# Performance work log

Measured on AMD Instinct MI355X. Metric: run time of the kernel, lower is better.

Reference implementation:

```python
import jax, jax.numpy as jnp
import numpy as np

N_NODES = 100000
N_EDGES = 1600000
HIDDEN = 128
N_ETYPES = 4
N_STEPS = 4


def setup_inputs() -> dict:
    key = jax.random.key(0)
    ks = jax.random.split(key, 10)
    s = 1.0 / np.sqrt(HIDDEN)
    node_feat = jax.random.normal(ks[0], (N_NODES, HIDDEN), dtype=jnp.float32)
    edge_index = jax.random.randint(ks[1], (2, N_EDGES), 0, N_NODES)
    edge_feat = jax.random.uniform(ks[2], (N_EDGES, N_ETYPES), dtype=jnp.float32)
    # per-edge-type linear layers (DGL GatedGraphConv uses nn.Linear per etype)
    W_edge = jax.random.uniform(ks[3], (N_ETYPES, HIDDEN, HIDDEN), minval=-s, maxval=s, dtype=jnp.float32)
    b_edge = jax.random.uniform(ks[4], (N_ETYPES, HIDDEN), minval=-s, maxval=s, dtype=jnp.float32)
    # GRUCell parameters (torch layout: gates stacked r, z, n)
    W_ih = jax.random.uniform(ks[5], (3 * HIDDEN, HIDDEN), minval=-s, maxval=s, dtype=jnp.float32)
    W_hh = jax.random.uniform(ks[6], (3 * HIDDEN, HIDDEN), minval=-s, maxval=s, dtype=jnp.float32)
    b_ih = jax.random.uniform(ks[7], (3 * HIDDEN,), minval=-s, maxval=s, dtype=jnp.float32)
    b_hh = jax.random.uniform(ks[8], (3 * HIDDEN,), minval=-s, maxval=s, dtype=jnp.float32)
    return {"node_feat": node_feat, "edge_index": edge_index, "edge_feat": edge_feat,
            "W_edge": W_edge, "b_edge": b_edge, "W_ih": W_ih, "W_hh": W_hh,
            "b_ih": b_ih, "b_hh": b_hh}


def _gru_cell(x, h, W_ih, W_hh, b_ih, b_hh):
    gi = x @ W_ih.T + b_ih  # (N, 3D)
    gh = h @ W_hh.T + b_hh
    ir, iz, inn = jnp.split(gi, 3, axis=1)
    hr, hz, hn = jnp.split(gh, 3, axis=1)
    r = jax.nn.sigmoid(ir + hr)
    z = jax.nn.sigmoid(iz + hz)
    n = jnp.tanh(inn + r * hn)
    return (1.0 - z) * n + z * h


def reference(node_feat, edge_index, edge_feat, W_edge, b_edge, W_ih, W_hh, b_ih, b_hh):
    etypes = jnp.argmax(edge_feat, axis=1)          # (E,)
    src, dst = edge_index[0], edge_index[1]
    N = node_feat.shape[0]
    h = node_feat
    for _ in range(N_STEPS):
        # per-etype linear transform of all nodes: (T, N, D)
        trans = jnp.einsum('nd,tod->tno', h, W_edge) + b_edge[:, None, :]
        msg = trans[etypes, src]                    # (E, D) gather by (etype, src)
        a = jax.ops.segment_sum(msg, dst, num_segments=N)  # scatter-add to dst
        h = _gru_cell(a, h, W_ih, W_hh, b_ih, b_hh)
    return h
```

## Files before the change

### kernel.cpp

```cpp
#include <hip/hip_runtime.h>

#define N_NODES 100000
#define N_EDGES 1600000
#define HID 128
#define SCAN_N (N_NODES*4)
#define NB1 ((SCAN_N + 1023) / 1024)
#define ZERO_IDX (N_NODES*4)

#define EB 8192
#define NBLKA ((N_EDGES + EB - 1) / EB)
#define BSH 9
#define NBUCK ((N_NODES + (1<<BSH) - 1) >> BSH)
#define N2 (NBUCK * NBLKA)
#define NB2 ((N2 + 1023) / 1024)

typedef __attribute__((ext_vector_type(8))) short short8;
typedef __attribute__((ext_vector_type(4))) float float4v;
typedef __attribute__((ext_vector_type(4))) int int4v;
typedef __attribute__((ext_vector_type(2))) unsigned int uint2v;
typedef unsigned short ushort_t;
typedef unsigned int uint_t;

__device__ __forceinline__ float bits2f(uint_t u){ union{uint_t u; float f;} x; x.u=u; return x.f; }
__device__ __forceinline__ float b2f(ushort_t u){ return bits2f(((uint_t)u)<<16); }
__device__ __forceinline__ ushort_t f2b(float f){
  union{float f; uint_t u;} x; x.f=f;
  uint_t r = x.u + 0x7fffu + ((x.u>>16)&1u);
  return (ushort_t)(r>>16);
}
__device__ __forceinline__ float sigm(float x){ return 1.0f/(1.0f+__expf(-x)); }
__device__ __forceinline__ float tanh_f(float x){
  float t=__expf(-2.0f*fabsf(x)); float y=(1.0f-t)/(1.0f+t); return x>=0.f? y : -y;
}
__device__ __forceinline__ int imin(int a, int b){ return a < b ? a : b; }


__global__ void prep_weights(const float* __restrict__ W_edge, const float* __restrict__ W_ih,
                             const float* __restrict__ W_hh, ushort_t* __restrict__ WY,
                             ushort_t* __restrict__ W2){
  int i = blockIdx.x*256 + threadIdx.x;
  if (i < 65536){
    WY[i] = f2b(W_edge[i]);
  } else if (i < 65536 + 131072){
    int i2 = i - 65536;
    int n_l = i2 >> 8, k = i2 & 255;
    int wn = n_l >> 7, j = (n_l >> 4) & 7, rr = n_l & 15;
    int c = wn*32 + (j&1)*16 + rr;
    int jg = j >> 1;
    float v;
    if (jg < 2)       v = (k < 128) ? W_ih[(jg*128 + c)*128 + k] : W_hh[(jg*128 + c)*128 + (k-128)];
    else if (jg == 2) v = (k < 128) ? W_ih[(256 + c)*128 + k] : 0.0f;
    else              v = (k >= 128) ? W_hh[(256 + c)*128 + (k-128)] : 0.0f;
    W2[n_l*256 + k] = f2b(v);
  }
}

__global__ void edge_pass1(const int* __restrict__ eidx, const float* __restrict__ efeat,
                           int* __restrict__ packed, int* __restrict__ cnt,
                           int* __restrict__ bcntT){
  __shared__ int hist[NBUCK];
  int tid = threadIdx.x, blk = blockIdx.x;
  for (int j = tid; j < NBUCK; j += 512) hist[j] = 0;
  __syncthreads();
  #pragma unroll
  for (int k = 0; k < EB/512; ++k){
    int e = blk*EB + k*512 + tid;
    if (e < N_EDGES){
      int src = eidx[e], dst = eidx[N_EDGES + e];
      float4v f = *(const float4v*)(efeat + (size_t)e*4);
      int t = 0; float b = f[0];
      if (f[1] > b){ b = f[1]; t = 1; }
      if (f[2] > b){ b = f[2]; t = 2; }
      if (f[3] > b){ b = f[3]; t = 3; }
      packed[e] = (src << 2) | t;
      atomicAdd(&cnt[dst*4 + t], 1);
      atomicAdd(&hist[dst >> BSH], 1);
    }
  }
  __syncthreads();
  for (int j = tid; j < NBUCK; j += 512) bcntT[j*NBLKA + blk] = hist[j];
}

__global__ void scan_pass1(const int* __restrict__ src, int* __restrict__ bsum, int n){
  __shared__ int ws[4];
  int tid = threadIdx.x, lane = tid & 63, w = tid >> 6;
  int idx = blockIdx.x*1024 + tid*4;
  int v = 0;
  if (idx + 3 < n){ int4v x = *(const int4v*)(src + idx); v = x[0]+x[1]+x[2]+x[3]; }
  else { for (int k = 0; k < 4; ++k) if (idx + k < n) v += src[idx+k]; }
  for (int d = 32; d; d >>= 1) v += __shfl_down(v, d);
  if (lane == 0) ws[w] = v;
  __syncthreads();
  if (tid == 0) bsum[blockIdx.x] = ws[0]+ws[1]+ws[2]+ws[3];
}

__global__ void scan_pass2(const int* __restrict__ bsum, int* __restrict__ bpre,
                           int* __restrict__ total_out, int nb){
  __shared__ int sh[512];
  int tid = threadIdx.x;
  int v = (tid < nb) ? bsum[tid] : 0;
  sh[tid] = v;
  __syncthreads();
  for (int d = 1; d < 512; d <<= 1){
    int y = (tid >= d) ? sh[tid-d] : 0;
    __syncthreads();
    sh[tid] += y;
    __syncthreads();
  }
  if (tid < nb) bpre[tid] = sh[tid] - v;
  if (tid == 511) *total_out = sh[511];
}

__global__ void scan_pass3(const int* __restrict__ src, const int* __restrict__ bpre,
                           int* __restrict__ off, int n){
  __shared__ int wsum[4];
  int tid = threadIdx.x, lane = tid & 63, w = tid >> 6;
  int idx = blockIdx.x*1024 + tid*4;
  int v0=0,v1=0,v2=0,v3=0;
  if (idx + 3 < n){ int4v x = *(const int4v*)(src + idx); v0=x[0];v1=x[1];v2=x[2];v3=x[3]; }
  else {
    if (idx   < n) v0 = src[idx];
    if (idx+1 < n) v1 = src[idx+1];
    if (idx+2 < n) v2 = src[idx+2];
    if (idx+3 < n) v3 = src[idx+3];
  }
  int ts = v0+v1+v2+v3;
  int sc = ts;
  for (int d = 1; d < 64; d <<= 1){ int y = __shfl_up(sc, d); if (lane >= d) sc += y; }
  if (lane == 63) wsum[w] = sc;
  __syncthreads();
  int wofs = 0;
  for (int k = 0; k < w; ++k) wofs += wsum[k];
  int base = bpre[blockIdx.x] + wofs + sc - ts;
  int e0 = base, e1 = e0+v0, e2 = e1+v1, e3 = e2+v2;
  if (idx   < n) off[idx  ] = e0;
  if (idx+1 < n) off[idx+1] = e1;
  if (idx+2 < n) off[idx+2] = e2;
  if (idx+3 < n) off[idx+3] = e3;
}

__global__ void bucket_scatter(const int* __restrict__ eidx, const int* __restrict__ packed,
                               const int* __restrict__ boffT, int* __restrict__ bucketed){
  __shared__ int cur[NBUCK];
  int tid = threadIdx.x, blk = blockIdx.x;
  for (int j = tid; j < NBUCK; j += 512) cur[j] = boffT[j*NBLKA + blk];
  __syncthreads();
  #pragma unroll
  for (int k = 0; k < EB/512; ++k){
    int e = blk*EB + k*512 + tid;
    if (e < N_EDGES){
      int dst = eidx[N_EDGES + e];
      int pos = atomicAdd(&cur[dst >> BSH], 1);
      bucketed[pos] = ((dst & ((1<<BSH)-1)) << 19) | packed[e];
    }
  }
}

__global__ void bucket_sort(const int* __restrict__ bucketed, const int* __restrict__ boffT,
                            const int* __restrict__ off4, int* __restrict__ sorted){
  __shared__ int cur[(1<<BSH)*4];
  int tid = threadIdx.x, b = blockIdx.x;
  int base = b * ((1<<BSH)*4);
  for (int j = tid; j < (1<<BSH)*4; j += 512)
    cur[j] = off4[imin(base + j, SCAN_N)];
  __syncthreads();
  int s = boffT[b*NBLKA];
  int e = boffT[(b+1)*NBLKA];
  for (int i = s + tid; i < e; i += 512){
    int w = bucketed[i];
    int ci = ((w >> 19) << 2) | (w & 3);
    int pos = atomicAdd(&cur[ci], 1);
    sorted[pos] = w & 0x7FFFF;
  }
}

__global__ void init_h(const float* __restrict__ nf, ushort_t* __restrict__ hB, int n4){
  int i = blockIdx.x*256 + threadIdx.x;
  if (i >= n4) return;
  float4v v = *(const float4v*)(nf + (size_t)i*4);
  uint2v u;
  u[0] = (uint_t)f2b(v[0]) | ((uint_t)f2b(v[1])<<16);
  u[1] = (uint_t)f2b(v[2]) | ((uint_t)f2b(v[3])<<16);
  *(uint2v*)(hB + (size_t)i*4) = u;
}


__launch_bounds__(512, 2)
__global__ void transform_kernel(const ushort_t* __restrict__ hB, const ushort_t* __restrict__ WY,
                                 ushort_t* __restrict__ Y){
  __shared__ ushort_t lA[128*64];
  __shared__ ushort_t lB[512*64];
  int tid = threadIdx.x, w = tid >> 6, lane = tid & 63;
  int wm = w >> 2, wn = w & 3;
  int row0 = blockIdx.x * 128;
  float4v acc[4][8] = {};
  for (int kt = 0; kt < 2; ++kt){
    short8 va[2], vb[8];
    #pragma unroll
    for (int i = 0; i < 2; ++i){
      int cidx = i*512 + tid;
      int r = cidx >> 3, ch = cidx & 7;
      int node = row0 + r; if (node >= N_NODES) node = N_NODES-1;
      va[i] = *reinterpret_cast<const short8*>(hB + (size_t)node*128 + kt*64 + ch*8);
    }
    #pragma unroll
    for (int i = 0; i < 8; ++i){
      int cidx = i*512 + tid;
      int n = cidx >> 3, ch = cidx & 7;
      vb[i] = *reinterpret_cast<const short8*>(WY + (size_t)n*128 + kt*64 + ch*8);
    }
    __syncthreads();
    #pragma unroll
    for (int i = 0; i < 2; ++i){
      int cidx = i*512 + tid;
      int r = cidx >> 3, ch = cidx & 7;
      *reinterpret_cast<short8*>(lA + r*64 + ((ch ^ (r&7))<<3)) = va[i];
    }
    #pragma unroll
    for (int i = 0; i < 8; ++i){
      int cidx = i*512 + tid;
      int n = cidx >> 3, ch = cidx & 7;
      *reinterpret_cast<short8*>(lB + n*64 + ((ch ^ (n&7))<<3)) = vb[i];
    }
    __syncthreads();
    #pragma unroll
    for (int kk = 0; kk < 2; ++kk){
      int lch = kk*4 + (lane>>4);
      short8 af[4], bf[8];
      #pragma unroll
      for (int i = 0; i < 4; ++i){
        int r = wm*64 + i*16 + (lane&15);
        af[i] = *reinterpret_cast<const short8*>(lA + r*64 + ((lch ^ (r&7))<<3));
      }
      #pragma unroll
      for (int j = 0; j < 8; ++j){
        int n = wn*128 + j*16 + (lane&15);
        bf[j] = *reinterpret_cast<const short8*>(lB + n*64 + ((lch ^ (n&7))<<3));
      }
      #pragma unroll
      for (int i = 0; i < 4; ++i)
        #pragma unroll
        for (int j = 0; j < 8; ++j)
          acc[i][j] = __builtin_amdgcn_mfma_f32_16x16x32_bf16(af[i], bf[j], acc[i][j], 0, 0, 0);
    }
    __syncthreads();
  }
  #pragma unroll
  for (int i = 0; i < 4; ++i)
    #pragma unroll
    for (int j = 0; j < 8; ++j)
      #pragma unroll
      for (int q = 0; q < 4; ++q){
        int grow = row0 + wm*64 + i*16 + (lane>>4)*4 + q;
        if (grow >= N_NODES) continue;
        int colc = wn*128 + j*16 + (lane&15);
        Y[(size_t)grow*512 + colc] = f2b(acc[i][j][q]);
      }
}

__global__ void agg_kernel(const int* __restrict__ off4, const int* __restrict__ sorted,
                           const ushort_t* __restrict__ Y, const int* __restrict__ cnt,
                           const float* __restrict__ b_edge, ushort_t* __restrict__ aB){
  int wid = (int)((blockIdx.x * blockDim.x + threadIdx.x) >> 6);
  int lane = threadIdx.x & 63;
  if (wid >= N_NODES) return;
  int s = off4[wid*4], e = off4[wid*4+4];
  int col = lane*2;
  float p0=0,p1=0,q0=0,q1=0,r0=0,r1=0,t0=0,t1=0;
  for (int i = s; i < e; i += 16){
    int vv[16];
    #pragma unroll
    for (int k = 0; k < 16; ++k){
      int j = i + k;
      int sv = sorted[imin(j, e-1)];
      vv[k] = __builtin_amdgcn_readfirstlane(j < e ? sv : ZERO_IDX);
    }
    uint_t hv[16];
    #pragma unroll
    for (int k = 0; k < 16; ++k)
      hv[k] = *(const uint_t*)(Y + (size_t)vv[k]*128 + col);
    #pragma unroll
    for (int k = 0; k < 16; ++k){
      float f0 = bits2f((hv[k] & 0xffffu) << 16);
      float f1 = bits2f(hv[k] & 0xffff0000u);
      if ((k&3)==0){ p0+=f0; p1+=f1; }
      else if ((k&3)==1){ q0+=f0; q1+=f1; }
      else if ((k&3)==2){ r0+=f0; r1+=f1; }
      else { t0+=f0; t1+=f1; }
    }
  }
  float s0 = (p0+q0)+(r0+t0);
  float s1 = (p1+q1)+(r1+t1);
  int4v c4 = *(const int4v*)(cnt + wid*4);
  #pragma unroll
  for (int t = 0; t < 4; ++t){
    float cf = (float)c4[t];
    s0 += cf * b_edge[t*128 + col];
    s1 += cf * b_edge[t*128 + col + 1];
  }
  *(uint_t*)(aB + (size_t)wid*128 + col) = (uint_t)f2b(s0) | ((uint_t)f2b(s1) << 16);
}

__launch_bounds__(512, 2)
__global__ void gru_kernel(const ushort_t* __restrict__ aB, ushort_t* __restrict__ hB,
                           const ushort_t* __restrict__ W2, const float* __restrict__ b_ih,
                           const float* __restrict__ b_hh, float* __restrict__ hF, int last){
  __shared__ ushort_t lA[128*64];
  __shared__ ushort_t lB[512*64];
  int tid = threadIdx.x, w = tid >> 6, lane = tid & 63;
  int wm = w >> 2, wn = w & 3;
  int row0 = blockIdx.x * 128;
  float4v acc[4][8] = {};
  for (int kt = 0; kt < 4; ++kt){
    short8 va[2], vb[8];
    const ushort_t* srcA = (kt < 2) ? aB : hB;
    #pragma unroll
    for (int i = 0; i < 2; ++i){
      int cidx = i*512 + tid;
      int r = cidx >> 3, ch = cidx & 7;
      int node = row0 + r; if (node >= N_NODES) node = N_NODES-1;
      va[i] = *reinterpret_cast<const short8*>(srcA + (size_t)node*128 + (kt&1)*64 + ch*8);
    }
    #pragma unroll
    for (int i = 0; i < 8; ++i){
      int cidx = i*512 + tid;
      int n = cidx >> 3, ch = cidx & 7;
      vb[i] = *reinterpret_cast<const short8*>(W2 + (size_t)n*256 + kt*64 + ch*8);
    }
    __syncthreads();
    #pragma unroll
    for (int i = 0; i < 2; ++i){
      int cidx = i*512 + tid;
      int r = cidx >> 3, ch = cidx & 7;
      *reinterpret_cast<short8*>(lA + r*64 + ((ch ^ (r&7))<<3)) = va[i];
    }
    #pragma unroll
    for (int i = 0; i < 8; ++i){
      int cidx = i*512 + tid;
      int n = cidx >> 3, ch = cidx & 7;
      *reinterpret_cast<short8*>(lB + n*64 + ((ch ^ (n&7))<<3)) = vb[i];
    }
    __syncthreads();
    #pragma unroll
    for (int kk = 0; kk < 2; ++kk){
      int lch = kk*4 + (lane>>4);
      short8 af[4], bf[8];
      #pragma unroll
      for (int i = 0; i < 4; ++i){
        int r = wm*64 + i*16 + (lane&15);
        af[i] = *reinterpret_cast<const short8*>(lA + r*64 + ((lch ^ (r&7))<<3));
      }
      #pragma unroll
      for (int j = 0; j < 8; ++j){
        int n = wn*128 + j*16 + (lane&15);
        bf[j] = *reinterpret_cast<const short8*>(lB + n*64 + ((lch ^ (n&7))<<3));
      }
      #pragma unroll
      for (int i = 0; i < 4; ++i)
        #pragma unroll
        for (int j = 0; j < 8; ++j)
          acc[i][j] = __builtin_amdgcn_mfma_f32_16x16x32_bf16(af[i], bf[j], acc[i][j], 0, 0, 0);
    }
    __syncthreads();
  }
  #pragma unroll
  for (int i = 0; i < 4; ++i){
    #pragma unroll
    for (int jj = 0; jj < 2; ++jj){
      int c = wn*32 + jj*16 + (lane&15);
      float br = b_ih[c] + b_hh[c];
      float bz = b_ih[128+c] + b_hh[128+c];
      float bni = b_ih[256+c], bnh = b_hh[256+c];
      #pragma unroll
      for (int q = 0; q < 4; ++q){
        int rrow = row0 + wm*64 + i*16 + (lane>>4)*4 + q;
        if (rrow >= N_NODES) continue;
        float rg = sigm(acc[i][0+jj][q] + br);
        float zg = sigm(acc[i][2+jj][q] + bz);
        float hn = acc[i][6+jj][q] + bnh;
        float nn = tanh_f(acc[i][4+jj][q] + bni + rg*hn);
        float h = b2f(hB[(size_t)rrow*128 + c]);
        float out = (1.0f - zg)*nn + zg*h;
        hB[(size_t)rrow*128 + c] = f2b(out);
        if (last) hF[(size_t)rrow*128 + c] = out;
      }
    }
  }
}


extern "C" void kernel_launch(void* const* d_in, const int* in_sizes, int n_in,
                              void* d_out, int out_size, void* d_ws, size_t ws_size,
                              hipStream_t stream) {
  const float* node_feat = (const float*)d_in[0];
  const int*   edge_idx  = (const int*)d_in[1];
  const float* edge_feat = (const float*)d_in[2];
  const float* W_edge    = (const float*)d_in[3];
  const float* b_edge    = (const float*)d_in[4];
  const float* W_ih      = (const float*)d_in[5];
  const float* W_hh      = (const float*)d_in[6];
  const float* b_ih      = (const float*)d_in[7];
  const float* b_hh      = (const float*)d_in[8];
  float* hF = (float*)d_out;

  char* p = (char*)d_ws;
  auto take = [&](size_t bytes) -> char* {
    char* r = p; p += (bytes + 255) & ~(size_t)255; return r;
  };
  ushort_t* WY     = (ushort_t*)take(512*128*2);
  ushort_t* W2     = (ushort_t*)take(512*256*2);
  int* cnt      = (int*)take((size_t)SCAN_N*4);
  int* off4     = (int*)take((size_t)(SCAN_N+1)*4);
  int* bcntT    = (int*)take((size_t)N2*4);
  int* boffT    = (int*)take((size_t)(N2+1)*4);
  int* bsum     = (int*)take(512*4);
  int* bpre     = (int*)take(512*4);
  int* packed   = (int*)take((size_t)N_EDGES*4);
  int* bucketed = (int*)take((size_t)N_EDGES*4);
  int* sorted   = (int*)take((size_t)N_EDGES*4);
  ushort_t* hB = (ushort_t*)take((size_t)N_NODES*128*2);
  ushort_t* Y  = (ushort_t*)take(((size_t)N_NODES*512 + 256)*2);
  ushort_t* aB = (ushort_t*)take((size_t)N_NODES*128*2);

  hipMemsetAsync(cnt, 0, (size_t)SCAN_N*4, stream);
  hipMemsetAsync(Y + (size_t)N_NODES*512, 0, 256*2, stream);

  prep_weights<<<768, 256, 0, stream>>>(W_edge, W_ih, W_hh, WY, W2);
  edge_pass1<<<NBLKA, 512, 0, stream>>>(edge_idx, edge_feat, packed, cnt, bcntT);
  scan_pass1<<<NB1, 256, 0, stream>>>(cnt, bsum, SCAN_N);
  scan_pass2<<<1, 512, 0, stream>>>(bsum, bpre, off4 + SCAN_N, NB1);
  scan_pass3<<<NB1, 256, 0, stream>>>(cnt, bpre, off4, SCAN_N);
  scan_pass1<<<NB2, 256, 0, stream>>>(bcntT, bsum, N2);
  scan_pass2<<<1, 512, 0, stream>>>(bsum, bpre, boffT + N2, NB2);
  scan_pass3<<<NB2, 256, 0, stream>>>(bcntT, bpre, boffT, N2);
  bucket_scatter<<<NBLKA, 512, 0, stream>>>(edge_idx, packed, boffT, bucketed);
  bucket_sort<<<NBUCK, 512, 0, stream>>>(bucketed, boffT, off4, sorted);
  init_h<<<(N_NODES*32 + 255)/256, 256, 0, stream>>>(node_feat, hB, N_NODES*32);

  int gemm_blocks = (N_NODES + 127) / 128;
  for (int step = 0; step < 4; ++step){
    transform_kernel<<<gemm_blocks, 512, 0, stream>>>(hB, WY, Y);
    agg_kernel<<<(N_NODES+3)/4, 256, 0, stream>>>(off4, sorted, Y, cnt, b_edge, aB);
    gru_kernel<<<gemm_blocks, 512, 0, stream>>>(aB, hB, W2, b_ih, b_hh, hF, step == 3);
  }
}
```

Before: 828.1 us.

## Stage GEMM epilogues through LDS for coalesced stores and skip zero-block MFMAs

The transform GEMM's epilogue now writes accumulators into shared memory and then issues 16-byte row-contiguous stores to Y, two column halves at a time. The old path made scattered 2-byte stores. The GRU GEMM skips loading B fragments and issuing MFMAs for weight blocks that are structurally zero: the n-gate input and hidden parts in the K halves that do not touch them. Its epilogue is also staged through LDS so hB and hF are written with vector stores. The final fp32 output is now rebuilt from the bf16-rounded value, so it loses precision. The first kernel's staging buffer (128x256 bf16) may exceed the original lB allocation.

```diff
diff --git a/kernel.cpp b/kernel.cpp
--- a/kernel.cpp
+++ b/kernel.cpp
@@ -246,16 +246,31 @@
     __syncthreads();
   }
   #pragma unroll
-  for (int i = 0; i < 4; ++i)
-    #pragma unroll
-    for (int j = 0; j < 8; ++j)
-      #pragma unroll
-      for (int q = 0; q < 4; ++q){
-        int grow = row0 + wm*64 + i*16 + (lane>>4)*4 + q;
-        if (grow >= N_NODES) continue;
-        int colc = wn*128 + j*16 + (lane&15);
-        Y[(size_t)grow*512 + colc] = f2b(acc[i][j][q]);
-      }
+  for (int h = 0; h < 2; ++h){
+    if (h) __syncthreads();
+    #pragma unroll
+    for (int i = 0; i < 4; ++i)
+      #pragma unroll
+      for (int jh = 0; jh < 4; ++jh)
+        #pragma unroll
+        for (int q = 0; q < 4; ++q){
+          int row = wm*64 + i*16 + (lane>>4)*4 + q;
+          int bc  = wn*64 + jh*16 + (lane&15);
+          lB[row*256 + bc] = f2b(acc[i][h*4+jh][q]);
+        }
+    __syncthreads();
+    #pragma unroll
+    for (int p = 0; p < 8; ++p){
+      int u = p*512 + tid;
+      int row = u >> 5, uc = u & 31;
+      int grow = row0 + row;
+      if (grow < N_NODES){
+        short8 v = *reinterpret_cast<const short8*>(lB + row*256 + uc*8);
+        int ycol = (uc>>3)*128 + h*64 + (uc&7)*8;
+        *reinterpret_cast<short8*>(Y + (size_t)grow*512 + ycol) = v;
+      }
+    }
+  }
 }
 
 __global__ void agg_kernel(const int* __restrict__ off4, const int* __restrict__ sorted,
@@ -341,6 +356,7 @@
       *reinterpret_cast<short8*>(lB + n*64 + ((ch ^ (n&7))<<3)) = vb[i];
     }
     __syncthreads();
+    bool lo = (kt < 2);
     #pragma unroll
     for (int kk = 0; kk < 2; ++kk){
       int lch = kk*4 + (lane>>4);
@@ -352,14 +368,13 @@
       }
       #pragma unroll
       for (int j = 0; j < 8; ++j){
+        if (lo ? (j >= 6) : (j == 4 || j == 5)) continue;
         int n = wn*128 + j*16 + (lane&15);
         bf[j] = *reinterpret_cast<const short8*>(lB + n*64 + ((lch ^ (n&7))<<3));
-      }
-      #pragma unroll
-      for (int i = 0; i < 4; ++i)
         #pragma unroll
-        for (int j = 0; j < 8; ++j)
+        for (int i = 0; i < 4; ++i)
           acc[i][j] = __builtin_amdgcn_mfma_f32_16x16x32_bf16(af[i], bf[j], acc[i][j], 0, 0, 0);
+      }
     }
     __syncthreads();
   }
@@ -373,16 +388,35 @@
       float bni = b_ih[256+c], bnh = b_hh[256+c];
       #pragma unroll
       for (int q = 0; q < 4; ++q){
-        int rrow = row0 + wm*64 + i*16 + (lane>>4)*4 + q;
-        if (rrow >= N_NODES) continue;
+        int row = wm*64 + i*16 + (lane>>4)*4 + q;
+        int rc = imin(row0 + row, N_NODES-1);
         float rg = sigm(acc[i][0+jj][q] + br);
         float zg = sigm(acc[i][2+jj][q] + bz);
         float hn = acc[i][6+jj][q] + bnh;
         float nn = tanh_f(acc[i][4+jj][q] + bni + rg*hn);
-        float h = b2f(hB[(size_t)rrow*128 + c]);
+        float h = b2f(hB[(size_t)rc*128 + c]);
         float out = (1.0f - zg)*nn + zg*h;
-        hB[(size_t)rrow*128 + c] = f2b(out);
-        if (last) hF[(size_t)rrow*128 + c] = out;
+        lB[row*128 + c] = f2b(out);
+      }
+    }
+  }
+  __syncthreads();
+  #pragma unroll
+  for (int p = 0; p < 4; ++p){
+    int u = p*512 + tid;
+    int row = u >> 4, uc = u & 15;
+    int grow = row0 + row;
+    if (grow < N_NODES){
+      short8 v = *reinterpret_cast<const short8*>(lB + row*128 + uc*8);
+      *reinterpret_cast<short8*>(hB + (size_t)grow*128 + uc*8) = v;
+      if (last){
+        float4v f0, f1;
+        #pragma unroll
+        for (int k = 0; k < 4; ++k) f0[k] = b2f((ushort_t)v[k]);
+        #pragma unroll
+        for (int k = 0; k < 4; ++k) f1[k] = b2f((ushort_t)v[4+k]);
+        *reinterpret_cast<float4v*>(hF + (size_t)grow*128 + uc*8)     = f0;
+        *reinterpret_cast<float4v*>(hF + (size_t)grow*128 + uc*8 + 4) = f1;
       }
     }
   }
```

After: 857.5 us. 3.5% more time.

## Drop LDS staging in GEMMs, load fragments directly, skip zero GRU blocks

Applied to the files above, without the earlier changes.

Transform and GRU GEMM kernels now have each wave load MFMA fragments directly from global memory with 64-row tiles, removing shared-memory staging and block barriers. GRU weights are re-laid out so each wave owns 16 output columns across all four gate blocks, and MFMAs on the structurally zero n-gate halves are skipped. This trades LDS reuse for more global/L2 traffic per wave and doubles the block count.

```diff
diff --git a/kernel.cpp b/kernel.cpp
--- a/kernel.cpp
+++ b/kernel.cpp
@@ -43,15 +43,14 @@
     WY[i] = f2b(W_edge[i]);
   } else if (i < 65536 + 131072){
     int i2 = i - 65536;
-    int n_l = i2 >> 8, k = i2 & 255;
-    int wn = n_l >> 7, j = (n_l >> 4) & 7, rr = n_l & 15;
-    int c = wn*32 + (j&1)*16 + rr;
-    int jg = j >> 1;
+    int n = i2 >> 8, k = i2 & 255;
+    int j = (n >> 4) & 3;
+    int c = ((n >> 6) << 4) | (n & 15);
     float v;
-    if (jg < 2)       v = (k < 128) ? W_ih[(jg*128 + c)*128 + k] : W_hh[(jg*128 + c)*128 + (k-128)];
-    else if (jg == 2) v = (k < 128) ? W_ih[(256 + c)*128 + k] : 0.0f;
-    else              v = (k >= 128) ? W_hh[(256 + c)*128 + (k-128)] : 0.0f;
-    W2[n_l*256 + k] = f2b(v);
+    if (j < 2)       v = (k < 128) ? W_ih[(j*128 + c)*128 + k] : W_hh[(j*128 + c)*128 + (k-128)];
+    else if (j == 2) v = (k < 128) ? W_ih[(256 + c)*128 + k] : 0.0f;
+    else             v = (k >= 128) ? W_hh[(256 + c)*128 + (k-128)] : 0.0f;
+    W2[n*256 + k] = f2b(v);
   }
 }
 
@@ -188,74 +187,38 @@
 __launch_bounds__(512, 2)
 __global__ void transform_kernel(const ushort_t* __restrict__ hB, const ushort_t* __restrict__ WY,
                                  ushort_t* __restrict__ Y){
-  __shared__ ushort_t lA[128*64];
-  __shared__ ushort_t lB[512*64];
   int tid = threadIdx.x, w = tid >> 6, lane = tid & 63;
-  int wm = w >> 2, wn = w & 3;
-  int row0 = blockIdx.x * 128;
-  float4v acc[4][8] = {};
-  for (int kt = 0; kt < 2; ++kt){
-    short8 va[2], vb[8];
-    #pragma unroll
-    for (int i = 0; i < 2; ++i){
-      int cidx = i*512 + tid;
-      int r = cidx >> 3, ch = cidx & 7;
-      int node = row0 + r; if (node >= N_NODES) node = N_NODES-1;
-      va[i] = *reinterpret_cast<const short8*>(hB + (size_t)node*128 + kt*64 + ch*8);
-    }
-    #pragma unroll
-    for (int i = 0; i < 8; ++i){
-      int cidx = i*512 + tid;
-      int n = cidx >> 3, ch = cidx & 7;
-      vb[i] = *reinterpret_cast<const short8*>(WY + (size_t)n*128 + kt*64 + ch*8);
-    }
-    __syncthreads();
-    #pragma unroll
-    for (int i = 0; i < 2; ++i){
-      int cidx = i*512 + tid;
-      int r = cidx >> 3, ch = cidx & 7;
-      *reinterpret_cast<short8*>(lA + r*64 + ((ch ^ (r&7))<<3)) = va[i];
-    }
-    #pragma unroll
-    for (int i = 0; i < 8; ++i){
-      int cidx = i*512 + tid;
-      int n = cidx >> 3, ch = cidx & 7;
-      *reinterpret_cast<short8*>(lB + n*64 + ((ch ^ (n&7))<<3)) = vb[i];
-    }
-    __syncthreads();
-    #pragma unroll
-    for (int kk = 0; kk < 2; ++kk){
-      int lch = kk*4 + (lane>>4);
-      short8 af[4], bf[8];
-      #pragma unroll
-      for (int i = 0; i < 4; ++i){
-        int r = wm*64 + i*16 + (lane&15);
-        af[i] = *reinterpret_cast<const short8*>(lA + r*64 + ((lch ^ (r&7))<<3));
-      }
-      #pragma unroll
-      for (int j = 0; j < 8; ++j){
-        int n = wn*128 + j*16 + (lane&15);
-        bf[j] = *reinterpret_cast<const short8*>(lB + n*64 + ((lch ^ (n&7))<<3));
-      }
+  int l15 = lane & 15, lq = lane >> 4;
+  int row0 = blockIdx.x * 64;
+  float4v acc[4][4] = {};
+  #pragma unroll
+  for (int s = 0; s < 4; ++s){
+    int klo = s*32 + lq*8;
+    short8 af[4];
+    #pragma unroll
+    for (int i = 0; i < 4; ++i){
+      int node = imin(row0 + i*16 + l15, N_NODES-1);
+      af[i] = *reinterpret_cast<const short8*>(hB + (size_t)node*128 + klo);
+    }
+    #pragma unroll
+    for (int j = 0; j < 4; ++j){
+      int n = w*64 + j*16 + l15;
+      short8 bf = *reinterpret_cast<const short8*>(WY + (size_t)n*128 + klo);
       #pragma unroll
       for (int i = 0; i < 4; ++i)
-        #pragma unroll
-        for (int j = 0; j < 8; ++j)
-          acc[i][j] = __builtin_amdgcn_mfma_f32_16x16x32_bf16(af[i], bf[j], acc[i][j], 0, 0, 0);
-    }
-    __syncthreads();
+        acc[i][j] = __builtin_amdgcn_mfma_f32_16x16x32_bf16(af[i], bf, acc[i][j], 0, 0, 0);
+    }
   }
   #pragma unroll
   for (int i = 0; i < 4; ++i)
     #pragma unroll
-    for (int j = 0; j < 8; ++j)
+    for (int q = 0; q < 4; ++q){
+      int grow = row0 + i*16 + lq*4 + q;
+      if (grow >= N_NODES) continue;
       #pragma unroll
-      for (int q = 0; q < 4; ++q){
-        int grow = row0 + wm*64 + i*16 + (lane>>4)*4 + q;
-        if (grow >= N_NODES) continue;
-        int colc = wn*128 + j*16 + (lane&15);
-        Y[(size_t)grow*512 + colc] = f2b(acc[i][j][q]);
-      }
+      for (int j = 0; j < 4; ++j)
+        Y[(size_t)grow*512 + w*64 + j*16 + l15] = f2b(acc[i][j][q]);
+    }
 }
 
 __global__ void agg_kernel(const int* __restrict__ off4, const int* __restrict__ sorted,
@@ -305,85 +268,49 @@
 __global__ void gru_kernel(const ushort_t* __restrict__ aB, ushort_t* __restrict__ hB,
                            const ushort_t* __restrict__ W2, const float* __restrict__ b_ih,
                            const float* __restrict__ b_hh, float* __restrict__ hF, int last){
-  __shared__ ushort_t lA[128*64];
-  __shared__ ushort_t lB[512*64];
   int tid = threadIdx.x, w = tid >> 6, lane = tid & 63;
-  int wm = w >> 2, wn = w & 3;
-  int row0 = blockIdx.x * 128;
-  float4v acc[4][8] = {};
-  for (int kt = 0; kt < 4; ++kt){
-    short8 va[2], vb[8];
-    const ushort_t* srcA = (kt < 2) ? aB : hB;
-    #pragma unroll
-    for (int i = 0; i < 2; ++i){
-      int cidx = i*512 + tid;
-      int r = cidx >> 3, ch = cidx & 7;
-      int node = row0 + r; if (node >= N_NODES) node = N_NODES-1;
-      va[i] = *reinterpret_cast<const short8*>(srcA + (size_t)node*128 + (kt&1)*64 + ch*8);
-    }
-    #pragma unroll
-    for (int i = 0; i < 8; ++i){
-      int cidx = i*512 + tid;
-      int n = cidx >> 3, ch = cidx & 7;
-      vb[i] = *reinterpret_cast<const short8*>(W2 + (size_t)n*256 + kt*64 + ch*8);
-    }
-    __syncthreads();
-    #pragma unroll
-    for (int i = 0; i < 2; ++i){
-      int cidx = i*512 + tid;
-      int r = cidx >> 3, ch = cidx & 7;
-      *reinterpret_cast<short8*>(lA + r*64 + ((ch ^ (r&7))<<3)) = va[i];
-    }
-    #pragma unroll
-    for (int i = 0; i < 8; ++i){
-      int cidx = i*512 + tid;
-      int n = cidx >> 3, ch = cidx & 7;
-      *reinterpret_cast<short8*>(lB + n*64 + ((ch ^ (n&7))<<3)) = vb[i];
-    }
-    __syncthreads();
-    #pragma unroll
-    for (int kk = 0; kk < 2; ++kk){
-      int lch = kk*4 + (lane>>4);
-      short8 af[4], bf[8];
-      #pragma unroll
-      for (int i = 0; i < 4; ++i){
-        int r = wm*64 + i*16 + (lane&15);
-        af[i] = *reinterpret_cast<const short8*>(lA + r*64 + ((lch ^ (r&7))<<3));
-      }
-      #pragma unroll
-      for (int j = 0; j < 8; ++j){
-        int n = wn*128 + j*16 + (lane&15);
-        bf[j] = *reinterpret_cast<const short8*>(lB + n*64 + ((lch ^ (n&7))<<3));
-      }
+  int l15 = lane & 15, lq = lane >> 4;
+  int row0 = blockIdx.x * 64;
+  float4v acc[4][4] = {};
+  #pragma unroll
+  for (int s = 0; s < 8; ++s){
+    const ushort_t* srcA = (s < 4) ? aB : hB;
+    int klo = (s & 3)*32 + lq*8;
+    short8 af[4];
+    #pragma unroll
+    for (int i = 0; i < 4; ++i){
+      int node = imin(row0 + i*16 + l15, N_NODES-1);
+      af[i] = *reinterpret_cast<const short8*>(srcA + (size_t)node*128 + klo);
+    }
+    #pragma unroll
+    for (int j = 0; j < 4; ++j){
+      if ((s < 4) ? (j == 3) : (j == 2)) continue;
+      int n = w*64 + j*16 + l15;
+      short8 bf = *reinterpret_cast<const short8*>(W2 + (size_t)n*256 + s*32 + lq*8);
       #pragma unroll
       for (int i = 0; i < 4; ++i)
-        #pragma unroll
-        for (int j = 0; j < 8; ++j)
-          acc[i][j] = __builtin_amdgcn_mfma_f32_16x16x32_bf16(af[i], bf[j], acc[i][j], 0, 0, 0);
-    }
-    __syncthreads();
-  }
+        acc[i][j] = __builtin_amdgcn_mfma_f32_16x16x32_bf16(af[i], bf, acc[i][j], 0, 0, 0);
+    }
+  }
+  int c = w*16 + l15;
+  float bir = b_ih[c]     + b_hh[c];
+  float biz = b_ih[128+c] + b_hh[128+c];
+  float bin = b_ih[256+c], bhn = b_hh[256+c];
+  __syncthreads();
   #pragma unroll
   for (int i = 0; i < 4; ++i){
     #pragma unroll
-    for (int jj = 0; jj < 2; ++jj){
-      int c = wn*32 + jj*16 + (lane&15);
-      float br = b_ih[c] + b_hh[c];
-      float bz = b_ih[128+c] + b_hh[128+c];
-      float bni = b_ih[256+c], bnh = b_hh[256+c];
-      #pragma unroll
-      for (int q = 0; q < 4; ++q){
-        int rrow = row0 + wm*64 + i*16 + (lane>>4)*4 + q;
-        if (rrow >= N_NODES) continue;
-        float rg = sigm(acc[i][0+jj][q] + br);
-        float zg = sigm(acc[i][2+jj][q] + bz);
-        float hn = acc[i][6+jj][q] + bnh;
-        float nn = tanh_f(acc[i][4+jj][q] + bni + rg*hn);
-        float h = b2f(hB[(size_t)rrow*128 + c]);
-        float out = (1.0f - zg)*nn + zg*h;
-        hB[(size_t)rrow*128 + c] = f2b(out);
-        if (last) hF[(size_t)rrow*128 + c] = out;
-      }
+    for (int q = 0; q < 4; ++q){
+      int grow = row0 + i*16 + lq*4 + q;
+      if (grow >= N_NODES) continue;
+      float rg = sigm(acc[i][0][q] + bir);
+      float zg = sigm(acc[i][1][q] + biz);
+      float hn = acc[i][3][q] + bhn;
+      float nn = tanh_f(acc[i][2][q] + bin + rg*hn);
+      float h = b2f(hB[(size_t)grow*128 + c]);
+      float out = (1.0f - zg)*nn + zg*h;
+      hB[(size_t)grow*128 + c] = f2b(out);
+      if (last) hF[(size_t)grow*128 + c] = out;
     }
   }
 }
@@ -437,10 +364,10 @@
   bucket_sort<<<NBUCK, 512, 0, stream>>>(bucketed, boffT, off4, sorted);
   init_h<<<(N_NODES*32 + 255)/256, 256, 0, stream>>>(node_feat, hB, N_NODES*32);
 
-  int gemm_blocks = (N_NODES + 127) / 128;
+  int gb = (N_NODES + 63) / 64;
   for (int step = 0; step < 4; ++step){
-    transform_kernel<<<gemm_blocks, 512, 0, stream>>>(hB, WY, Y);
+    transform_kernel<<<gb, 512, 0, stream>>>(hB, WY, Y);
     agg_kernel<<<(N_NODES+3)/4, 256, 0, stream>>>(off4, sorted, Y, cnt, b_edge, aB);
-    gru_kernel<<<gemm_blocks, 512, 0, stream>>>(aB, hB, W2, b_ih, b_hh, hF, step == 3);
-  }
-}
+    gru_kernel<<<gb, 512, 0, stream>>>(aB, hB, W2, b_ih, b_hh, hF, step == 3);
+  }
+}
```

After: 1.123 ms. 1.36x slower.

## Fuse next-step edge-type transform into GRU kernel and skip zero gate blocks

Applied to the files above, without the earlier changes.

The GRU kernel now stages its new hidden-state tile in shared memory and immediately multiplies it by the per-edge-type weights to produce Y for the next step. This removes the separate transform launch on steps 1-3 and the global re-read of h. It also skips the MFMAs for the gate blocks that are structurally zero: the n-input block on the h half of K, and the n-hidden block on the a half. The cost is more shared-memory reuse, extra syncs and a longer kernel body per block.

```diff
diff --git a/kernel.cpp b/kernel.cpp
--- a/kernel.cpp
+++ b/kernel.cpp
@@ -302,89 +302,154 @@
 }
 
 __launch_bounds__(512, 2)
-__global__ void gru_kernel(const ushort_t* __restrict__ aB, ushort_t* __restrict__ hB,
-                           const ushort_t* __restrict__ W2, const float* __restrict__ b_ih,
-                           const float* __restrict__ b_hh, float* __restrict__ hF, int last){
+__global__ void gru_tr_kernel(const ushort_t* __restrict__ aB, ushort_t* __restrict__ hB,
+                              const ushort_t* __restrict__ W2, const ushort_t* __restrict__ WY,
+                              const float* __restrict__ b_ih, const float* __restrict__ b_hh,
+                              float* __restrict__ hF, ushort_t* __restrict__ Y, int last){
   __shared__ ushort_t lA[128*64];
   __shared__ ushort_t lB[512*64];
   int tid = threadIdx.x, w = tid >> 6, lane = tid & 63;
   int wm = w >> 2, wn = w & 3;
+  int l15 = lane & 15, lq = lane >> 4;
   int row0 = blockIdx.x * 128;
-  float4v acc[4][8] = {};
-  for (int kt = 0; kt < 4; ++kt){
-    short8 va[2], vb[8];
-    const ushort_t* srcA = (kt < 2) ? aB : hB;
-    #pragma unroll
-    for (int i = 0; i < 2; ++i){
-      int cidx = i*512 + tid;
-      int r = cidx >> 3, ch = cidx & 7;
-      int node = row0 + r; if (node >= N_NODES) node = N_NODES-1;
-      va[i] = *reinterpret_cast<const short8*>(srcA + (size_t)node*128 + (kt&1)*64 + ch*8);
-    }
-    #pragma unroll
-    for (int i = 0; i < 8; ++i){
-      int cidx = i*512 + tid;
-      int n = cidx >> 3, ch = cidx & 7;
-      vb[i] = *reinterpret_cast<const short8*>(W2 + (size_t)n*256 + kt*64 + ch*8);
-    }
-    __syncthreads();
-    #pragma unroll
-    for (int i = 0; i < 2; ++i){
-      int cidx = i*512 + tid;
-      int r = cidx >> 3, ch = cidx & 7;
-      *reinterpret_cast<short8*>(lA + r*64 + ((ch ^ (r&7))<<3)) = va[i];
-    }
-    #pragma unroll
-    for (int i = 0; i < 8; ++i){
-      int cidx = i*512 + tid;
-      int n = cidx >> 3, ch = cidx & 7;
-      *reinterpret_cast<short8*>(lB + n*64 + ((ch ^ (n&7))<<3)) = vb[i];
-    }
-    __syncthreads();
-    #pragma unroll
-    for (int kk = 0; kk < 2; ++kk){
-      int lch = kk*4 + (lane>>4);
-      short8 af[4], bf[8];
+  {
+    float4v acc[4][8] = {};
+    for (int kt = 0; kt < 4; ++kt){
+      short8 va[2], vb[8];
+      const ushort_t* srcA = (kt < 2) ? aB : hB;
+      #pragma unroll
+      for (int i = 0; i < 2; ++i){
+        int cidx = i*512 + tid;
+        int r = cidx >> 3, ch = cidx & 7;
+        int node = row0 + r; if (node >= N_NODES) node = N_NODES-1;
+        va[i] = *reinterpret_cast<const short8*>(srcA + (size_t)node*128 + (kt&1)*64 + ch*8);
+      }
+      #pragma unroll
+      for (int i = 0; i < 8; ++i){
+        int cidx = i*512 + tid;
+        int n = cidx >> 3, ch = cidx & 7;
+        vb[i] = *reinterpret_cast<const short8*>(W2 + (size_t)n*256 + kt*64 + ch*8);
+      }
+      __syncthreads();
+      #pragma unroll
+      for (int i = 0; i < 2; ++i){
+        int cidx = i*512 + tid;
+        int r = cidx >> 3, ch = cidx & 7;
+        *reinterpret_cast<short8*>(lA + r*64 + ((ch ^ (r&7))<<3)) = va[i];
+      }
+      #pragma unroll
+      for (int i = 0; i < 8; ++i){
+        int cidx = i*512 + tid;
+        int n = cidx >> 3, ch = cidx & 7;
+        *reinterpret_cast<short8*>(lB + n*64 + ((ch ^ (n&7))<<3)) = vb[i];
+      }
+      __syncthreads();
+      bool lo = (kt < 2);
+      #pragma unroll
+      for (int kk = 0; kk < 2; ++kk){
+        int lch = kk*4 + lq;
+        short8 af[4], bf[8];
+        #pragma unroll
+        for (int i = 0; i < 4; ++i){
+          int r = wm*64 + i*16 + l15;
+          af[i] = *reinterpret_cast<const short8*>(lA + r*64 + ((lch ^ (r&7))<<3));
+        }
+        #pragma unroll
+        for (int j = 0; j < 8; ++j){
+          if (lo ? (j >= 6) : (j == 4 || j == 5)) continue;
+          int n = wn*128 + j*16 + l15;
+          bf[j] = *reinterpret_cast<const short8*>(lB + n*64 + ((lch ^ (n&7))<<3));
+          #pragma unroll
+          for (int i = 0; i < 4; ++i)
+            acc[i][j] = __builtin_amdgcn_mfma_f32_16x16x32_bf16(af[i], bf[j], acc[i][j], 0, 0, 0);
+        }
+      }
+      __syncthreads();
+    }
+    #pragma unroll
+    for (int i = 0; i < 4; ++i){
+      #pragma unroll
+      for (int jj = 0; jj < 2; ++jj){
+        int c = wn*32 + jj*16 + l15;
+        float bir = b_ih[c] + b_hh[c];
+        float biz = b_ih[128+c] + b_hh[128+c];
+        float bni = b_ih[256+c], bnh = b_hh[256+c];
+        int ch = c >> 3;
+        #pragma unroll
+        for (int q = 0; q < 4; ++q){
+          int row = wm*64 + i*16 + lq*4 + q;
+          int grow = row0 + row;
+          float rg = sigm(acc[i][0+jj][q] + bir);
+          float zg = sigm(acc[i][2+jj][q] + biz);
+          float hn = acc[i][6+jj][q] + bnh;
+          float nn = tanh_f(acc[i][4+jj][q] + bni + rg*hn);
+          int rc = imin(grow, N_NODES-1);
+          float h = b2f(hB[(size_t)rc*128 + c]);
+          float out = (1.0f - zg)*nn + zg*h;
+          ushort_t ob = f2b(out);
+          lB[16384 + row*128 + ((ch ^ (row&15))<<3) + (c&7)] = ob;
+          if (grow < N_NODES){
+            hB[(size_t)grow*128 + c] = ob;
+            if (last) hF[(size_t)grow*128 + c] = out;
+          }
+        }
+      }
+    }
+  }
+  if (last) return;
+  __syncthreads();
+  #pragma unroll
+  for (int nh = 0; nh < 2; ++nh){
+    float4v acc2[4][4] = {};
+    #pragma unroll
+    for (int kt = 0; kt < 2; ++kt){
+      short8 vw[4];
       #pragma unroll
       for (int i = 0; i < 4; ++i){
-        int r = wm*64 + i*16 + (lane&15);
-        af[i] = *reinterpret_cast<const short8*>(lA + r*64 + ((lch ^ (r&7))<<3));
-      }
-      #pragma unroll
-      for (int j = 0; j < 8; ++j){
-        int n = wn*128 + j*16 + (lane&15);
-        bf[j] = *reinterpret_cast<const short8*>(lB + n*64 + ((lch ^ (n&7))<<3));
-      }
-      #pragma unroll
-      for (int i = 0; i < 4; ++i)
-        #pragma unroll
-        for (int j = 0; j < 8; ++j)
-          acc[i][j] = __builtin_amdgcn_mfma_f32_16x16x32_bf16(af[i], bf[j], acc[i][j], 0, 0, 0);
-    }
-    __syncthreads();
-  }
-  #pragma unroll
-  for (int i = 0; i < 4; ++i){
-    #pragma unroll
-    for (int jj = 0; jj < 2; ++jj){
-      int c = wn*32 + jj*16 + (lane&15);
-      float br = b_ih[c] + b_hh[c];
-      float bz = b_ih[128+c] + b_hh[128+c];
-      float bni = b_ih[256+c], bnh = b_hh[256+c];
+        int cidx = i*512 + tid;
+        int n = cidx >> 3, ch = cidx & 7;
+        vw[i] = *reinterpret_cast<const short8*>(WY + (size_t)(nh*256 + n)*128 + kt*64 + ch*8);
+      }
+      __syncthreads();
+      #pragma unroll
+      for (int i = 0; i < 4; ++i){
+        int cidx = i*512 + tid;
+        int n = cidx >> 3, ch = cidx & 7;
+        *reinterpret_cast<short8*>(lB + n*64 + ((ch ^ (n&7))<<3)) = vw[i];
+      }
+      __syncthreads();
+      #pragma unroll
+      for (int kk = 0; kk < 2; ++kk){
+        int lchh = kt*8 + kk*4 + lq;
+        int lchw = kk*4 + lq;
+        short8 af[4], bf[4];
+        #pragma unroll
+        for (int i = 0; i < 4; ++i){
+          int r = wm*64 + i*16 + l15;
+          af[i] = *reinterpret_cast<const short8*>(lB + 16384 + r*128 + ((lchh ^ (r&15))<<3));
+        }
+        #pragma unroll
+        for (int j = 0; j < 4; ++j){
+          int n = wn*64 + j*16 + l15;
+          bf[j] = *reinterpret_cast<const short8*>(lB + n*64 + ((lchw ^ (n&7))<<3));
+        }
+        #pragma unroll
+        for (int i = 0; i < 4; ++i)
+          #pragma unroll
+          for (int j = 0; j < 4; ++j)
+            acc2[i][j] = __builtin_amdgcn_mfma_f32_16x16x32_bf16(af[i], bf[j], acc2[i][j], 0, 0, 0);
+      }
+    }
+    #pragma unroll
+    for (int i = 0; i < 4; ++i)
       #pragma unroll
       for (int q = 0; q < 4; ++q){
-        int rrow = row0 + wm*64 + i*16 + (lane>>4)*4 + q;
-        if (rrow >= N_NODES) continue;
-        float rg = sigm(acc[i][0+jj][q] + br);
-        float zg = sigm(acc[i][2+jj][q] + bz);
-        float hn = acc[i][6+jj][q] + bnh;
-        float nn = tanh_f(acc[i][4+jj][q] + bni + rg*hn);
-        float h = b2f(hB[(size_t)rrow*128 + c]);
-        float out = (1.0f - zg)*nn + zg*h;
-        hB[(size_t)rrow*128 + c] = f2b(out);
-        if (last) hF[(size_t)rrow*128 + c] = out;
-      }
-    }
+        int grow = row0 + wm*64 + i*16 + lq*4 + q;
+        if (grow >= N_NODES) continue;
+        #pragma unroll
+        for (int j = 0; j < 4; ++j)
+          Y[(size_t)grow*512 + nh*256 + wn*64 + j*16 + l15] = f2b(acc2[i][j][q]);
+      }
   }
 }
 
@@ -437,10 +502,10 @@
   bucket_sort<<<NBUCK, 512, 0, stream>>>(bucketed, boffT, off4, sorted);
   init_h<<<(N_NODES*32 + 255)/256, 256, 0, stream>>>(node_feat, hB, N_NODES*32);
 
-  int gemm_blocks = (N_NODES + 127) / 128;
+  int gb = (N_NODES + 127) / 128;
+  transform_kernel<<<gb, 512, 0, stream>>>(hB, WY, Y);
   for (int step = 0; step < 4; ++step){
-    transform_kernel<<<gemm_blocks, 512, 0, stream>>>(hB, WY, Y);
     agg_kernel<<<(N_NODES+3)/4, 256, 0, stream>>>(off4, sorted, Y, cnt, b_edge, aB);
-    gru_kernel<<<gemm_blocks, 512, 0, stream>>>(aB, hB, W2, b_ih, b_hh, hF, step == 3);
-  }
-}
+    gru_tr_kernel<<<gb, 512, 0, stream>>>(aB, hB, W2, WY, b_ih, b_hh, hF, Y, step == 3);
+  }
+}
```

New measurement: 805.9 us. 1.03x faster.
